# Optimization experiments

Measured on AMD Instinct MI355X. Metric: run time of the kernel, lower is better.

The kernel has to match this reference:

```python
import jax, jax.numpy as jnp
import numpy as np

N_NODES = 10000
N_EDGES = 80000
F_IN = 128
H1 = 2048
H2 = 2048
H3 = 1024


def _sgconv(x, pos, src, dst, W_in, b_in, W_out, b_out):
    # geo-GCN SpatialGraphConv with hidden_size=1:
    # message(j->i) = relu(Linear(pos_j - pos_i)) * x_j ; aggr='add' ; then Linear out
    rel = pos[src] - pos[dst]                      # [E, 2]  (pos_j - pos_i)
    scale = jax.nn.relu(rel @ W_in + b_in)         # [E, C_in]
    msg = scale * x[src]                           # [E, C_in]
    agg = jax.ops.segment_sum(msg, dst, num_segments=x.shape[0])  # [N, C_in]
    return agg @ W_out + b_out                     # [N, C_out]


def setup_inputs() -> dict:
    key = jax.random.key(0)
    ks = jax.random.split(key, 12)
    x = jax.random.normal(ks[0], (N_NODES, F_IN), dtype=jnp.float32)
    pos = jax.random.normal(ks[1], (N_NODES, 2), dtype=jnp.float32)
    edge_index = jax.random.randint(ks[2], (2, N_EDGES), 0, N_NODES, dtype=jnp.int32)

    def lin(k, fan_in, fan_out):
        lim = 1.0 / np.sqrt(fan_in)
        kw, kb = jax.random.split(k)
        W = jax.random.uniform(kw, (fan_in, fan_out), jnp.float32, -lim, lim)
        b = jax.random.uniform(kb, (fan_out,), jnp.float32, -lim, lim)
        return W, b

    W_in1, b_in1 = lin(ks[3], 2, F_IN)
    W_out1, b_out1 = lin(ks[4], F_IN, H1)
    W_in2, b_in2 = lin(ks[5], 2, H1)
    W_out2, b_out2 = lin(ks[6], H1, H2)
    W_in3, b_in3 = lin(ks[7], 2, H2)
    W_out3, b_out3 = lin(ks[8], H2, H3)

    return {
        "x": x, "pos": pos, "edge_index": edge_index,
        "W_in1": W_in1, "b_in1": b_in1, "W_out1": W_out1, "b_out1": b_out1,
        "W_in2": W_in2, "b_in2": b_in2, "W_out2": W_out2, "b_out2": b_out2,
        "W_in3": W_in3, "b_in3": b_in3, "W_out3": W_out3, "b_out3": b_out3,
    }


def reference(x, pos, edge_index,
              W_in1, b_in1, W_out1, b_out1,
              W_in2, b_in2, W_out2, b_out2,
              W_in3, b_in3, W_out3, b_out3):
    src, dst = edge_index[0], edge_index[1]  # flow source_to_target: j=src, i=dst
    h = jax.nn.relu(_sgconv(x, pos, src, dst, W_in1, b_in1, W_out1, b_out1))
    h = jax.nn.relu(_sgconv(h, pos, src, dst, W_in2, b_in2, W_out2, b_out2))
    h = jax.nn.relu(_sgconv(h, pos, src, dst, W_in3, b_in3, W_out3, b_out3))
    # F.normalize(h, dim=1): L2 normalize rows with eps clamp 1e-12
    norm = jnp.linalg.norm(h, axis=1, keepdims=True)
    return h / jnp.maximum(norm, 1e-12)
```

## Files before the change

### kernel.cpp

```cpp
#include <hip/hip_runtime.h>
#include <hip/hip_bf16.h>

#define DEVI __device__ __forceinline__

constexpr int NN = 10000;
constexpr int NE = 80000;
constexpr int AGG_ROWS = 10240;
constexpr int ES_CAP = 110016;

typedef __attribute__((ext_vector_type(8))) short bf16x8;
typedef __attribute__((ext_vector_type(4))) float f32x4;

DEVI float blo(unsigned int u) {
  union { unsigned int i; float f; } c; c.i = u << 16; return c.f;
}
DEVI float bhi(unsigned int u) {
  union { unsigned int i; float f; } c; c.i = u & 0xffff0000u; return c.f;
}
DEVI unsigned short f2b(float f) {
  union { float f; unsigned int i; } c; c.f = f;
  unsigned int i = c.i;
  return (unsigned short)((i + 0x7fffu + ((i >> 16) & 1u)) >> 16);
}
DEVI void st1(float* p, float v) { *p = v; }
DEVI void st1(unsigned short* p, float v) { *p = f2b(v); }
DEVI void store8b(unsigned short* p, const float v[8]) {
  int4 pk;
  pk.x = (int)((unsigned)f2b(v[0]) | ((unsigned)f2b(v[1]) << 16));
  pk.y = (int)((unsigned)f2b(v[2]) | ((unsigned)f2b(v[3]) << 16));
  pk.z = (int)((unsigned)f2b(v[4]) | ((unsigned)f2b(v[5]) << 16));
  pk.w = (int)((unsigned)f2b(v[6]) | ((unsigned)f2b(v[7]) << 16));
  *reinterpret_cast<int4*>(p) = pk;
}

DEVI void gload16(const void* g, void* l) {
  __builtin_amdgcn_global_load_lds(
      (const __attribute__((address_space(1))) void*)g,
      (__attribute__((address_space(3))) void*)l, 16, 0, 0);
}

__global__ __launch_bounds__(256)
void hist_kernel(const int* __restrict__ dst, int* __restrict__ cnt) {
  int e = blockIdx.x * 256 + threadIdx.x;
  if (e < NE) atomicAdd(&cnt[dst[e]], 1);
}

__global__ __launch_bounds__(1024)
void scan_kernel(const int* __restrict__ cnt, int* __restrict__ off,
                 int* __restrict__ cursor) {
  __shared__ int wpart[16];
  __shared__ int carry;
  int tid = threadIdx.x, lane = tid & 63, w = tid >> 6;
  if (tid == 0) carry = 0;
  __syncthreads();
  for (int base = 0; base < NN; base += 1024) {
    int i = base + tid;
    int v = (i < NN) ? ((cnt[i] + 3) & ~3) : 0;
    int s = v;
#pragma unroll
    for (int o = 1; o < 64; o <<= 1) { int t = __shfl_up(s, o); if (lane >= o) s += t; }
    if (lane == 63) wpart[w] = s;
    __syncthreads();
    if (w == 0) {
      int ws = (lane < 16) ? wpart[lane] : 0;
#pragma unroll
      for (int o = 1; o < 16; o <<= 1) { int t = __shfl_up(ws, o); if (lane >= o) ws += t; }
      if (lane < 16) wpart[lane] = ws;
    }
    __syncthreads();
    int ex = carry + (w ? wpart[w - 1] : 0) + s - v;
    if (i < NN) { off[i] = ex; cursor[i] = ex; }
    __syncthreads();
    if (tid == 0) carry += wpart[15];
    __syncthreads();
  }
}

__global__ __launch_bounds__(256)
void bucket_kernel(const int* __restrict__ src, const int* __restrict__ dst,
                   const float* __restrict__ pos,
                   int* __restrict__ cursor, int* __restrict__ es,
                   float* __restrict__ rel) {
  int e = blockIdx.x * 256 + threadIdx.x;
  if (e < NE) {
    int s = src[e], d = dst[e];
    int p = atomicAdd(&cursor[d], 1);
    float2 ps = *reinterpret_cast<const float2*>(pos + 2 * s);
    float2 pd = *reinterpret_cast<const float2*>(pos + 2 * d);
    es[p] = s;
    *reinterpret_cast<float2*>(rel + 2 * p) = make_float2(ps.x - pd.x, ps.y - pd.y);
  }
}

__global__ __launch_bounds__(256)
void transpose_w(const float* __restrict__ W, unsigned short* __restrict__ WT,
                 int K, int N) {
  __shared__ float tile[32][33];
  int tx = threadIdx.x & 31, ty = threadIdx.x >> 5;
  int n0 = blockIdx.x * 32, k0 = blockIdx.y * 32;
#pragma unroll
  for (int j = 0; j < 32; j += 8)
    tile[ty + j][tx] = W[(size_t)(k0 + ty + j) * N + n0 + tx];
  __syncthreads();
#pragma unroll
  for (int j = 0; j < 32; j += 8)
    WT[(size_t)(n0 + ty + j) * K + k0 + tx] = f2b(tile[tx][ty + j]);
}

__global__ __launch_bounds__(256)
void gather_l1(const float* __restrict__ x,
               const int* __restrict__ off, const int* __restrict__ cnt,
               const int* __restrict__ es, const float* __restrict__ rel,
               const float* __restrict__ Win, const float* __restrict__ bin,
               unsigned short* __restrict__ agg) {
  constexpr int C = 128;
  int lane = threadIdx.x & 63;
  int i = blockIdx.x * 4 + (threadIdx.x >> 6);
  if (i >= NN) return;
  int c = lane * 2;
  float w00 = Win[c], w01 = Win[c + 1];
  float w10 = Win[C + c], w11 = Win[C + c + 1];
  float b0 = bin[c], b1 = bin[c + 1];
  float a0 = 0.f, a1 = 0.f;
  int s0 = off[i], n = cnt[i];

  for (int k = 0; k < n; k += 4) {
    int4 s4 = *reinterpret_cast<const int4*>(es + s0 + k);
    float4 ra = *reinterpret_cast<const float4*>(rel + 2 * (s0 + k));
    float4 rb = *reinterpret_cast<const float4*>(rel + 2 * (s0 + k) + 4);
    float2 q0 = *reinterpret_cast<const float2*>(x + (size_t)s4.x * C + c);
    float2 q1 = *reinterpret_cast<const float2*>(x + (size_t)s4.y * C + c);
    float2 q2 = *reinterpret_cast<const float2*>(x + (size_t)s4.z * C + c);
    float2 q3 = *reinterpret_cast<const float2*>(x + (size_t)s4.w * C + c);
    {
      float sc0 = fmaxf(fmaf(ra.x, w00, fmaf(ra.y, w10, b0)), 0.f);
      float sc1 = fmaxf(fmaf(ra.x, w01, fmaf(ra.y, w11, b1)), 0.f);
      a0 = fmaf(sc0, q0.x, a0); a1 = fmaf(sc1, q0.y, a1);
    }
    if (k + 1 < n) {
      float sc0 = fmaxf(fmaf(ra.z, w00, fmaf(ra.w, w10, b0)), 0.f);
      float sc1 = fmaxf(fmaf(ra.z, w01, fmaf(ra.w, w11, b1)), 0.f);
      a0 = fmaf(sc0, q1.x, a0); a1 = fmaf(sc1, q1.y, a1);
    }
    if (k + 2 < n) {
      float sc0 = fmaxf(fmaf(rb.x, w00, fmaf(rb.y, w10, b0)), 0.f);
      float sc1 = fmaxf(fmaf(rb.x, w01, fmaf(rb.y, w11, b1)), 0.f);
      a0 = fmaf(sc0, q2.x, a0); a1 = fmaf(sc1, q2.y, a1);
    }
    if (k + 3 < n) {
      float sc0 = fmaxf(fmaf(rb.z, w00, fmaf(rb.w, w10, b0)), 0.f);
      float sc1 = fmaxf(fmaf(rb.z, w01, fmaf(rb.w, w11, b1)), 0.f);
      a0 = fmaf(sc0, q3.x, a0); a1 = fmaf(sc1, q3.y, a1);
    }
  }
  unsigned int pk = (unsigned)f2b(a0) | ((unsigned)f2b(a1) << 16);
  *reinterpret_cast<unsigned int*>(agg + (size_t)i * C + c) = pk;
}

__global__ __launch_bounds__(256)
void gather_chunk(const unsigned short* __restrict__ x,
                  const int* __restrict__ off, const int* __restrict__ cnt,
                  const int* __restrict__ es, const float* __restrict__ rel,
                  const float* __restrict__ Win, const float* __restrict__ bin,
                  unsigned short* __restrict__ agg, int ngb8) {
  constexpr int C = 2048;
  constexpr int V = 8;
  int wgid = blockIdx.x;
  int half = wgid >= ngb8;
  int base = half ? wgid - ngb8 : wgid;
  int chunk = (base & 7) + (half << 3);
  int grp = base >> 3;
  int lane = threadIdx.x & 63;
  int wid = threadIdx.x >> 6;
  int slot = lane >> 4;
  int l16 = lane & 15;
  int i = grp * 16 + wid * 4 + slot;
  int c = chunk * 128 + l16 * V;

  float w0[V], w1[V], bb[V], acc[V];
#pragma unroll
  for (int j = 0; j < V; ++j) {
    w0[j] = Win[c + j]; w1[j] = Win[C + c + j]; bb[j] = bin[c + j]; acc[j] = 0.f;
  }
  int s0 = off[i], n = cnt[i];

  auto fma8 = [&](float rx, float ry, const int4& q) {
    float xv[V] = { blo(q.x), bhi(q.x), blo(q.y), bhi(q.y),
                    blo(q.z), bhi(q.z), blo(q.w), bhi(q.w) };
#pragma unroll
    for (int j = 0; j < V; ++j) {
      float sc = fmaxf(fmaf(rx, w0[j], fmaf(ry, w1[j], bb[j])), 0.f);
      acc[j] = fmaf(sc, xv[j], acc[j]);
    }
  };
  for (int k = 0; k < n; k += 4) {
    int4 s4 = *reinterpret_cast<const int4*>(es + s0 + k);
    float4 ra = *reinterpret_cast<const float4*>(rel + 2 * (s0 + k));
    float4 rb = *reinterpret_cast<const float4*>(rel + 2 * (s0 + k) + 4);
    int4 q0 = *reinterpret_cast<const int4*>(x + (size_t)s4.x * C + c);
    int4 q1 = *reinterpret_cast<const int4*>(x + (size_t)s4.y * C + c);
    int4 q2 = *reinterpret_cast<const int4*>(x + (size_t)s4.z * C + c);
    int4 q3 = *reinterpret_cast<const int4*>(x + (size_t)s4.w * C + c);
    fma8(ra.x, ra.y, q0);
    if (k + 1 < n) fma8(ra.z, ra.w, q1);
    if (k + 2 < n) fma8(rb.x, rb.y, q2);
    if (k + 3 < n) fma8(rb.z, rb.w, q3);
  }
  store8b(agg + (size_t)i * C + c, acc);
}

template <typename OT>
__global__ __launch_bounds__(512, 4)
void gemm320(const unsigned short* __restrict__ A,
             const unsigned short* __restrict__ BT,
             const float* __restrict__ bias, OT* __restrict__ out,
             int M, int N, int K) {
  __shared__ unsigned short lds[2 * 14336];
  const int t = threadIdx.x;
  const int lane = t & 63, wid = t >> 6;
  const int wr = wid >> 1, wc = wid & 1;

  const int nwg = gridDim.x * gridDim.y;
  const int orig = blockIdx.y * gridDim.x + blockIdx.x;
  const int swz = (orig & 7) * (nwg >> 3) + (orig >> 3);
  const int bx = swz % gridDim.x, by = swz / gridDim.x;
  const int m0 = by * 320, n0 = bx * 128;
  const int nk = K >> 5;

  const int lrow = lane >> 2;
  const int schunk = (lane & 3) ^ ((lrow >> 1) & 3);
  const bool isA = wid < 4;
  const int aw = wid & 3;
  const unsigned short* gSrc = isA
      ? A + (size_t)(m0 + aw * 80 + lrow) * K + schunk * 8
      : BT + (size_t)(n0 + aw * 32 + lrow) * K + schunk * 8;
  const int lBase = isA ? (aw * 5 * 512 + lane * 8)
                        : (10240 + aw * 2 * 512 + lane * 8);

  auto STAGE = [&](int buf, int kt) {
    const unsigned short* g = gSrc + kt * 32;
    unsigned short* l = lds + buf * 14336 + lBase;
    if (isA) {
#pragma unroll
      for (int jj = 0; jj < 5; ++jj)
        gload16(g + (size_t)(jj * 16) * K, l + jj * 512);
    } else {
#pragma unroll
      for (int jj = 0; jj < 2; ++jj)
        gload16(g + (size_t)(jj * 16) * K, l + jj * 512);
    }
  };

  const int frow = lane & 15;
  const int fslot = ((lane >> 4) ^ ((frow >> 1) & 3)) * 8;
  const int paOff = (wr * 80 + frow) * 32 + fslot;
  const int pbOff = 10240 + (wc * 64 + frow) * 32 + fslot;

  f32x4 acc[5][4];
#pragma unroll
  for (int m = 0; m < 5; ++m)
#pragma unroll
    for (int n = 0; n < 4; ++n) acc[m][n] = 0.f;

  STAGE(0, 0);

  int cur = 0;
  for (int kt = 0; kt < nk; ++kt) {
    if (kt + 1 < nk) {
      STAGE(cur ^ 1, kt + 1);
      if (isA) asm volatile("s_waitcnt vmcnt(5)" ::: "memory");
      else     asm volatile("s_waitcnt vmcnt(2)" ::: "memory");
    } else {
      asm volatile("s_waitcnt vmcnt(0)" ::: "memory");
    }
    asm volatile("s_barrier" ::: "memory");
    const unsigned short* pa = lds + cur * 14336 + paOff;
    const unsigned short* pb = lds + cur * 14336 + pbOff;
    bf16x8 bf[4];
#pragma unroll
    for (int n = 0; n < 4; ++n)
      bf[n] = *reinterpret_cast<const bf16x8*>(pb + n * 512);
    __builtin_amdgcn_s_setprio(1);
#pragma unroll
    for (int m = 0; m < 5; ++m) {
      bf16x8 af = *reinterpret_cast<const bf16x8*>(pa + m * 512);
#pragma unroll
      for (int n = 0; n < 4; ++n)
        acc[m][n] = __builtin_amdgcn_mfma_f32_16x16x32_bf16(
            af, bf[n], acc[m][n], 0, 0, 0);
    }
    __builtin_amdgcn_s_setprio(0);
    asm volatile("s_barrier" ::: "memory");
    cur ^= 1;
  }

  const int ccol = lane & 15;
  const int crow = (lane >> 4) * 4;
  float bv[4];
#pragma unroll
  for (int n = 0; n < 4; ++n)
    bv[n] = bias[n0 + wc * 64 + n * 16 + ccol];
#pragma unroll
  for (int m = 0; m < 5; ++m) {
    int gm0 = m0 + wr * 80 + m * 16 + crow;
#pragma unroll
    for (int r = 0; r < 4; ++r) {
      int gm = gm0 + r;
      if (gm < M) {
        size_t base = (size_t)gm * N + n0 + wc * 64 + ccol;
#pragma unroll
        for (int n = 0; n < 4; ++n)
          st1(out + base + n * 16, fmaxf(acc[m][n][r] + bv[n], 0.f));
      }
    }
  }
}

template <typename OT>
__global__ __launch_bounds__(256, 2)
void gemm160(const unsigned short* __restrict__ A,
             const unsigned short* __restrict__ BT,
             const float* __restrict__ bias, OT* __restrict__ out,
             int M, int N, int K) {
  extern __shared__ unsigned short lds[];
  const int t = threadIdx.x;
  const int lane = t & 63, wid = t >> 6;
  const int wr = wid >> 1, wc = wid & 1;

  const int nwg = gridDim.x * gridDim.y;
  const int orig = blockIdx.y * gridDim.x + blockIdx.x;
  const int swz = (orig & 7) * (nwg >> 3) + (orig >> 3);
  const int bx = swz % gridDim.x, by = swz / gridDim.x;
  const int m0 = by * 160, n0 = bx * 128;
  const int nk = K >> 6;

  const int lrow = lane >> 3;
  const int schunk = (lane & 7) ^ lrow;
  const unsigned short* gA = A + (size_t)(m0 + wid * 40 + lrow) * K + schunk * 8;
  const unsigned short* gB = BT + (size_t)(n0 + wid * 32 + lrow) * K + schunk * 8;
  unsigned short* lA = lds + (wid * 5) * 512 + lane * 8;
  unsigned short* lB = lds + 20480 + (wid * 4) * 512 + lane * 8;

  auto STAGE = [&](int buf, int kt) {
    const size_t ko = (size_t)kt << 6;
#pragma unroll
    for (int jj = 0; jj < 5; ++jj)
      gload16(gA + (size_t)(jj * 8) * K + ko, lA + buf * 10240 + jj * 512);
#pragma unroll
    for (int jj = 0; jj < 4; ++jj)
      gload16(gB + (size_t)(jj * 8) * K + ko, lB + buf * 8192 + jj * 512);
  };

  const int frow = lane & 15;
  const int fr7 = frow & 7;
  const int slot0 = ((lane >> 4) ^ fr7) * 8;
  const int slot1 = ((4 + (lane >> 4)) ^ fr7) * 8;
  const int paRow = (wr * 80 + frow) * 64;
  const int pbRow = (wc * 64 + frow) * 64;

  f32x4 acc[5][4];
#pragma unroll
  for (int m = 0; m < 5; ++m)
#pragma unroll
    for (int n = 0; n < 4; ++n) acc[m][n] = 0.f;

  STAGE(0, 0);

  int cur = 0;
  for (int kt = 0; kt < nk; ++kt) {
    if (kt + 1 < nk) {
      STAGE(cur ^ 1, kt + 1);
      asm volatile("s_waitcnt vmcnt(9)" ::: "memory");
    } else {
      asm volatile("s_waitcnt vmcnt(0)" ::: "memory");
    }
    asm volatile("s_barrier" ::: "memory");
    const unsigned short* pa = lds + cur * 10240 + paRow;
    const unsigned short* pb = lds + 20480 + cur * 8192 + pbRow;
#pragma unroll
    for (int ks = 0; ks < 2; ++ks) {
      const int sl = ks ? slot1 : slot0;
      bf16x8 af[5], bf[4];
#pragma unroll
      for (int m = 0; m < 5; ++m)
        af[m] = *reinterpret_cast<const bf16x8*>(pa + m * 1024 + sl);
#pragma unroll
      for (int n = 0; n < 4; ++n)
        bf[n] = *reinterpret_cast<const bf16x8*>(pb + n * 1024 + sl);
      __builtin_amdgcn_s_setprio(1);
#pragma unroll
      for (int m = 0; m < 5; ++m)
#pragma unroll
        for (int n = 0; n < 4; ++n)
          acc[m][n] = __builtin_amdgcn_mfma_f32_16x16x32_bf16(
              af[m], bf[n], acc[m][n], 0, 0, 0);
      __builtin_amdgcn_s_setprio(0);
    }
    asm volatile("s_barrier" ::: "memory");
    cur ^= 1;
  }

  const int ccol = lane & 15;
  const int crow = (lane >> 4) * 4;
  float bv[4];
#pragma unroll
  for (int n = 0; n < 4; ++n)
    bv[n] = bias[n0 + wc * 64 + n * 16 + ccol];
#pragma unroll
  for (int m = 0; m < 5; ++m) {
    int gm0 = m0 + wr * 80 + m * 16 + crow;
#pragma unroll
    for (int r = 0; r < 4; ++r) {
      int gm = gm0 + r;
      if (gm < M) {
        size_t base = (size_t)gm * N + n0 + wc * 64 + ccol;
#pragma unroll
        for (int n = 0; n < 4; ++n)
          st1(out + base + n * 16, fmaxf(acc[m][n][r] + bv[n], 0.f));
      }
    }
  }
}

__global__ __launch_bounds__(256)
void l2norm_kernel(float* __restrict__ out) {
  constexpr int C = 1024;
  float* p = out + (size_t)blockIdx.x * C;
  float4 v = *reinterpret_cast<const float4*>(p + threadIdx.x * 4);
  float s = v.x * v.x + v.y * v.y + v.z * v.z + v.w * v.w;
#pragma unroll
  for (int o = 32; o > 0; o >>= 1) s += __shfl_down(s, o);
  __shared__ float wsum[4];
  if ((threadIdx.x & 63) == 0) wsum[threadIdx.x >> 6] = s;
  __syncthreads();
  float tot = wsum[0] + wsum[1] + wsum[2] + wsum[3];
  float inv = 1.0f / fmaxf(sqrtf(tot), 1e-12f);
  float4 r = make_float4(v.x * inv, v.y * inv, v.z * inv, v.w * inv);
  *reinterpret_cast<float4*>(p + threadIdx.x * 4) = r;
}

extern "C" void kernel_launch(void* const* d_in, const int* in_sizes, int n_in,
                              void* d_out, int out_size, void* d_ws, size_t ws_size,
                              hipStream_t stream) {
  (void)in_sizes; (void)n_in; (void)out_size; (void)ws_size;
  const float* x     = (const float*)d_in[0];
  const float* pos   = (const float*)d_in[1];
  const int*   ei    = (const int*)d_in[2];
  const int*   srcv  = ei;
  const int*   dstv  = ei + NE;
  const float* Win1  = (const float*)d_in[3];
  const float* bin1  = (const float*)d_in[4];
  const float* Wout1 = (const float*)d_in[5];
  const float* bout1 = (const float*)d_in[6];
  const float* Win2  = (const float*)d_in[7];
  const float* bin2  = (const float*)d_in[8];
  const float* Wout2 = (const float*)d_in[9];
  const float* bout2 = (const float*)d_in[10];
  const float* Win3  = (const float*)d_in[11];
  const float* bin3  = (const float*)d_in[12];
  const float* Wout3 = (const float*)d_in[13];
  const float* bout3 = (const float*)d_in[14];
  float* outp = (float*)d_out;

  char* ws = (char*)d_ws;
  unsigned short* aggb = (unsigned short*)ws;
  unsigned short* h1   = (unsigned short*)(ws + 41943040);
  unsigned short* W2T  = (unsigned short*)(ws + 82903040);
  unsigned short* W3T  = (unsigned short*)(ws + 91291648);
  unsigned short* W1T  = (unsigned short*)(ws + 95485952);
  int* cnt    = (int*)(ws + 96010240);
  int* off    = (int*)(ws + 96050240);
  int* cursor = (int*)(ws + 96090240);
  int* es     = (int*)(ws + 96130240);
  float* rel  = (float*)(ws + 96570304);
  unsigned short* h2 = (unsigned short*)d_out;

  hipFuncSetAttribute((const void*)gemm160<float>,
                      hipFuncAttributeMaxDynamicSharedMemorySize, 73728);

  const dim3 blk(256);
  const int eb = (NE + 255) / 256;
  const int ngb8 = ((NN + 15) / 16) * 8;

  hipMemsetAsync(cnt, 0, NN * sizeof(int), stream);
  hipMemsetAsync(es, 0, ES_CAP * sizeof(int), stream);
  hist_kernel<<<eb, blk, 0, stream>>>(dstv, cnt);
  scan_kernel<<<1, 1024, 0, stream>>>(cnt, off, cursor);
  bucket_kernel<<<eb, blk, 0, stream>>>(srcv, dstv, pos, cursor, es, rel);

  transpose_w<<<dim3(2048 / 32, 128 / 32),  blk, 0, stream>>>(Wout1, W1T, 128, 2048);
  transpose_w<<<dim3(2048 / 32, 2048 / 32), blk, 0, stream>>>(Wout2, W2T, 2048, 2048);
  transpose_w<<<dim3(1024 / 32, 2048 / 32), blk, 0, stream>>>(Wout3, W3T, 2048, 1024);

  hipMemsetAsync(aggb + (size_t)NN * 2048, 0, (size_t)(AGG_ROWS - NN) * 2048 * 2, stream);

  gather_l1<<<(NN + 3) / 4, blk, 0, stream>>>(x, off, cnt, es, rel, Win1, bin1, aggb);
  gemm320<unsigned short><<<dim3(2048 / 128, AGG_ROWS / 320), 512, 0, stream>>>(
      aggb, W1T, bout1, h1, NN, 2048, 128);

  gather_chunk<<<2 * ngb8, blk, 0, stream>>>(h1, off, cnt, es, rel, Win2, bin2, aggb, ngb8);
  gemm320<unsigned short><<<dim3(2048 / 128, AGG_ROWS / 320), 512, 0, stream>>>(
      aggb, W2T, bout2, h2, NN, 2048, 2048);

  gather_chunk<<<2 * ngb8, blk, 0, stream>>>(h2, off, cnt, es, rel, Win3, bin3, aggb, ngb8);
  gemm160<float><<<dim3(1024 / 128, AGG_ROWS / 160), blk, 73728, stream>>>(
      aggb, W3T, bout3, outp, NN, 1024, 2048);

  l2norm_kernel<<<NN, blk, 0, stream>>>(outp);
}
```

Before: 311.9 us.

## Replace 320x128 GEMM with 320x256 tile using 32x32x16 MFMA and BK=64

Layers 1 and 2 now use a new GEMM kernel. It has a 320x256 block tile, a K-step of 64 staged into 144KB of dynamic LDS, and 32x32x16 bf16 MFMA instructions in place of 16x16x32. Each wave computes a 160x64 sub-tile. The aim is to raise arithmetic intensity per LDS and global load and to cut barrier overhead per FLOP. In exchange, occupancy drops to one block per CU because of the LDS size, and the grid becomes smaller (256 blocks), which may leave CUs underused.

```diff
diff --git a/kernel.cpp b/kernel.cpp
--- a/kernel.cpp
+++ b/kernel.cpp
@@ -10,6 +10,7 @@
 
 typedef __attribute__((ext_vector_type(8))) short bf16x8;
 typedef __attribute__((ext_vector_type(4))) float f32x4;
+typedef __attribute__((ext_vector_type(16))) float f32x16;
 
 DEVI float blo(unsigned int u) {
   union { unsigned int i; float f; } c; c.i = u << 16; return c.f;
@@ -210,57 +211,52 @@
 }
 
 template <typename OT>
-__global__ __launch_bounds__(512, 4)
-void gemm320(const unsigned short* __restrict__ A,
-             const unsigned short* __restrict__ BT,
-             const float* __restrict__ bias, OT* __restrict__ out,
-             int M, int N, int K) {
-  __shared__ unsigned short lds[2 * 14336];
+__global__ __launch_bounds__(512, 2)
+void gemm3232(const unsigned short* __restrict__ A,
+              const unsigned short* __restrict__ BT,
+              const float* __restrict__ bias, OT* __restrict__ out,
+              int M, int N, int K) {
+  extern __shared__ unsigned short lds[];
   const int t = threadIdx.x;
   const int lane = t & 63, wid = t >> 6;
-  const int wr = wid >> 1, wc = wid & 1;
+  const int wr = wid >> 2, wc = wid & 3;
 
   const int nwg = gridDim.x * gridDim.y;
   const int orig = blockIdx.y * gridDim.x + blockIdx.x;
   const int swz = (orig & 7) * (nwg >> 3) + (orig >> 3);
   const int bx = swz % gridDim.x, by = swz / gridDim.x;
-  const int m0 = by * 320, n0 = bx * 128;
-  const int nk = K >> 5;
-
-  const int lrow = lane >> 2;
-  const int schunk = (lane & 3) ^ ((lrow >> 1) & 3);
-  const bool isA = wid < 4;
-  const int aw = wid & 3;
-  const unsigned short* gSrc = isA
-      ? A + (size_t)(m0 + aw * 80 + lrow) * K + schunk * 8
-      : BT + (size_t)(n0 + aw * 32 + lrow) * K + schunk * 8;
-  const int lBase = isA ? (aw * 5 * 512 + lane * 8)
-                        : (10240 + aw * 2 * 512 + lane * 8);
+  const int m0 = by * 320, n0 = bx * 256;
+  const int nk = K >> 6;
+
+  const int srow = t >> 3;
+  const int schunk = (t & 7) ^ (srow & 7);
+  const unsigned short* gA = A + (size_t)(m0 + srow) * K + schunk * 8;
+  const unsigned short* gB = BT + (size_t)(n0 + srow) * K + schunk * 8;
+  const int lt8 = t * 8;
 
   auto STAGE = [&](int buf, int kt) {
-    const unsigned short* g = gSrc + kt * 32;
-    unsigned short* l = lds + buf * 14336 + lBase;
-    if (isA) {
-#pragma unroll
-      for (int jj = 0; jj < 5; ++jj)
-        gload16(g + (size_t)(jj * 16) * K, l + jj * 512);
-    } else {
-#pragma unroll
-      for (int jj = 0; jj < 2; ++jj)
-        gload16(g + (size_t)(jj * 16) * K, l + jj * 512);
-    }
+    const size_t ko = (size_t)kt << 6;
+    unsigned short* lb = lds + buf * 36864;
+#pragma unroll
+    for (int jj = 0; jj < 5; ++jj)
+      gload16(gA + (size_t)(jj * 64) * K + ko, lb + jj * 4096 + lt8);
+#pragma unroll
+    for (int jj = 0; jj < 4; ++jj)
+      gload16(gB + (size_t)(jj * 64) * K + ko, lb + 20480 + jj * 4096 + lt8);
   };
 
-  const int frow = lane & 15;
-  const int fslot = ((lane >> 4) ^ ((frow >> 1) & 3)) * 8;
-  const int paOff = (wr * 80 + frow) * 32 + fslot;
-  const int pbOff = 10240 + (wc * 64 + frow) * 32 + fslot;
-
-  f32x4 acc[5][4];
+  const int frow32 = lane & 31, cb = lane >> 5;
+  const int fr7 = frow32 & 7;
+  const int paRow = (wr * 160 + frow32) * 64;
+  const int pbRow = 20480 + (wc * 64 + frow32) * 64;
+
+  f32x16 acc[5][2];
 #pragma unroll
   for (int m = 0; m < 5; ++m)
 #pragma unroll
-    for (int n = 0; n < 4; ++n) acc[m][n] = 0.f;
+    for (int n = 0; n < 2; ++n)
+#pragma unroll
+      for (int r = 0; r < 16; ++r) acc[m][n][r] = 0.f;
 
   STAGE(0, 0);
 
@@ -268,49 +264,53 @@
   for (int kt = 0; kt < nk; ++kt) {
     if (kt + 1 < nk) {
       STAGE(cur ^ 1, kt + 1);
-      if (isA) asm volatile("s_waitcnt vmcnt(5)" ::: "memory");
-      else     asm volatile("s_waitcnt vmcnt(2)" ::: "memory");
+      asm volatile("s_waitcnt vmcnt(9)" ::: "memory");
     } else {
       asm volatile("s_waitcnt vmcnt(0)" ::: "memory");
     }
     asm volatile("s_barrier" ::: "memory");
-    const unsigned short* pa = lds + cur * 14336 + paOff;
-    const unsigned short* pb = lds + cur * 14336 + pbOff;
-    bf16x8 bf[4];
-#pragma unroll
-    for (int n = 0; n < 4; ++n)
-      bf[n] = *reinterpret_cast<const bf16x8*>(pb + n * 512);
-    __builtin_amdgcn_s_setprio(1);
-#pragma unroll
-    for (int m = 0; m < 5; ++m) {
-      bf16x8 af = *reinterpret_cast<const bf16x8*>(pa + m * 512);
-#pragma unroll
-      for (int n = 0; n < 4; ++n)
-        acc[m][n] = __builtin_amdgcn_mfma_f32_16x16x32_bf16(
-            af, bf[n], acc[m][n], 0, 0, 0);
-    }
-    __builtin_amdgcn_s_setprio(0);
+    const unsigned short* pa = lds + cur * 36864 + paRow;
+    const unsigned short* pb = lds + cur * 36864 + pbRow;
+#pragma unroll
+    for (int ks = 0; ks < 4; ++ks) {
+      const int sl = (((ks << 1) | cb) ^ fr7) * 8;
+      bf16x8 af[5], bf[2];
+#pragma unroll
+      for (int n = 0; n < 2; ++n)
+        bf[n] = *reinterpret_cast<const bf16x8*>(pb + n * 2048 + sl);
+#pragma unroll
+      for (int m = 0; m < 5; ++m)
+        af[m] = *reinterpret_cast<const bf16x8*>(pa + m * 2048 + sl);
+      __builtin_amdgcn_s_setprio(1);
+#pragma unroll
+      for (int m = 0; m < 5; ++m)
+#pragma unroll
+        for (int n = 0; n < 2; ++n)
+          acc[m][n] = __builtin_amdgcn_mfma_f32_32x32x16_bf16(
+              af[m], bf[n], acc[m][n], 0, 0, 0);
+      __builtin_amdgcn_s_setprio(0);
+    }
     asm volatile("s_barrier" ::: "memory");
     cur ^= 1;
   }
 
-  const int ccol = lane & 15;
-  const int crow = (lane >> 4) * 4;
-  float bv[4];
-#pragma unroll
-  for (int n = 0; n < 4; ++n)
-    bv[n] = bias[n0 + wc * 64 + n * 16 + ccol];
+  const int ccol = lane & 31;
+  const int crow4 = (lane >> 5) * 4;
+  float bv[2];
+#pragma unroll
+  for (int n = 0; n < 2; ++n)
+    bv[n] = bias[n0 + wc * 64 + n * 32 + ccol];
 #pragma unroll
   for (int m = 0; m < 5; ++m) {
-    int gm0 = m0 + wr * 80 + m * 16 + crow;
-#pragma unroll
-    for (int r = 0; r < 4; ++r) {
-      int gm = gm0 + r;
+    const int gmBase = m0 + wr * 160 + m * 32 + crow4;
+#pragma unroll
+    for (int r = 0; r < 16; ++r) {
+      int gm = gmBase + (r & 3) + 8 * (r >> 2);
       if (gm < M) {
         size_t base = (size_t)gm * N + n0 + wc * 64 + ccol;
 #pragma unroll
-        for (int n = 0; n < 4; ++n)
-          st1(out + base + n * 16, fmaxf(acc[m][n][r] + bv[n], 0.f));
+        for (int n = 0; n < 2; ++n)
+          st1(out + base + n * 32, fmaxf(acc[m][n][r] + bv[n], 0.f));
       }
     }
   }
@@ -475,6 +475,8 @@
   float* rel  = (float*)(ws + 96570304);
   unsigned short* h2 = (unsigned short*)d_out;
 
+  hipFuncSetAttribute((const void*)gemm3232<unsigned short>,
+                      hipFuncAttributeMaxDynamicSharedMemorySize, 147456);
   hipFuncSetAttribute((const void*)gemm160<float>,
                       hipFuncAttributeMaxDynamicSharedMemorySize, 73728);
 
@@ -495,11 +497,11 @@
   hipMemsetAsync(aggb + (size_t)NN * 2048, 0, (size_t)(AGG_ROWS - NN) * 2048 * 2, stream);
 
   gather_l1<<<(NN + 3) / 4, blk, 0, stream>>>(x, off, cnt, es, rel, Win1, bin1, aggb);
-  gemm320<unsigned short><<<dim3(2048 / 128, AGG_ROWS / 320), 512, 0, stream>>>(
+  gemm3232<unsigned short><<<dim3(2048 / 256, AGG_ROWS / 320), 512, 147456, stream>>>(
       aggb, W1T, bout1, h1, NN, 2048, 128);
 
   gather_chunk<<<2 * ngb8, blk, 0, stream>>>(h1, off, cnt, es, rel, Win2, bin2, aggb, ngb8);
-  gemm320<unsigned short><<<dim3(2048 / 128, AGG_ROWS / 320), 512, 0, stream>>>(
+  gemm3232<unsigned short><<<dim3(2048 / 256, AGG_ROWS / 320), 512, 147456, stream>>>(
       aggb, W2T, bout2, h2, NN, 2048, 2048);
 
   gather_chunk<<<2 * ngb8, blk, 0, stream>>>(h2, off, cnt, es, rel, Win3, bin3, aggb, ngb8);
```

New measurement: 317.7 us. About the same (+1.9%).
